# Optimization experiments

Hardware: AMD Instinct MI355X
Metric: run time of the kernel (lower is better)

## Reference

```python
import jax, jax.numpy as jnp
import numpy as np

KH, KW = 5, 5            # local window (h, w), must be odd
SIGMA = 1.0
GAUSS_DEN = 2.0 * SIGMA ** 2
N, C, H, W = 4, 20, 64, 2048


def setup_inputs() -> dict:
    key = jax.random.key(0)
    k1, k2, k3 = jax.random.split(key, 3)
    xyz = jax.random.normal(k1, (N, 3, H, W), dtype=jnp.float32)
    softmax = jax.random.uniform(k2, (N, C, H, W), dtype=jnp.float32)
    mask = jax.random.randint(k3, (N, H, W), 0, 2).astype(jnp.bool_)
    return {"xyz": xyz, "softmax": softmax, "mask": mask}


def reference(xyz, softmax, mask):
    # xyz: [N,3,H,W], softmax: [N,C,H,W], mask: [N,H,W]
    sm = softmax * mask[:, None].astype(softmax.dtype)
    ph, pw = KH // 2, KW // 2
    # zero padding matches F.unfold's implicit zero padding
    xyz_p = jnp.pad(xyz, ((0, 0), (0, 0), (ph, ph), (pw, pw)))
    sm_p = jnp.pad(sm, ((0, 0), (0, 0), (ph, ph), (pw, pw)))
    out = jnp.zeros_like(sm)
    # Fused form of the im2col math: for each window offset, weight the
    # shifted (masked) softmax by the XYZ-distance Gaussian and accumulate.
    # 25 static offsets -> small fixed unrolled loop, no giant unfold buffers.
    for dy in range(KH):
        for dx in range(KW):
            wxyz = xyz_p[:, :, dy:dy + sm.shape[2], dx:dx + sm.shape[3]]  # [N,3,H,W]
            d2 = jnp.sum((wxyz - xyz) ** 2, axis=1)                       # [N,H,W]
            g = jnp.exp(-d2 / GAUSS_DEN)                                  # [N,H,W]
            out = out + g[:, None] * sm_p[:, :, dy:dy + sm.shape[2], dx:dx + sm.shape[3]]
    return out
```

## Files before the change

kernel.cpp:

```cpp
#include <hip/hip_runtime.h>

#define NN 4
#define CC 20
#define HH 64
#define WW 2048
#define CG 4
#define CPG (CC / CG)
#define PX 4

__global__ __launch_bounds__(256, 4) void lc_xyz_kernel(
    const float* __restrict__ xyz,
    const float* __restrict__ softmax,
    const int* __restrict__ mask,
    float* __restrict__ out)
{
    const int t  = blockIdx.x * blockDim.x + threadIdx.x;
    const int h  = blockIdx.y;
    const int nz = blockIdx.z;
    const int n  = nz >> 2;
    const int cg = nz & 3;
    const int hw = HH * WW;
    const int p0 = t * PX;

    const float* xb  = xyz     + (size_t)n * 3  * hw;
    const float* smb = softmax + (size_t)n * CC * hw + (size_t)(cg * CPG) * hw;
    const int*   mb  = mask    + (size_t)n * hw;

    const int ctr = h * WW + p0;
    const float4 cxv = *(const float4*)(xb + 0 * hw + ctr);
    const float4 cyv = *(const float4*)(xb + 1 * hw + ctr);
    const float4 czv = *(const float4*)(xb + 2 * hw + ctr);
    const float cx[PX] = {cxv.x, cxv.y, cxv.z, cxv.w};
    const float cy[PX] = {cyv.x, cyv.y, cyv.z, cyv.w};
    const float cz[PX] = {czv.x, czv.y, czv.z, czv.w};

    float acc[CPG][PX];
#pragma unroll
    for (int c = 0; c < CPG; ++c)
#pragma unroll
        for (int i = 0; i < PX; ++i) acc[c][i] = 0.f;

    int c0 = p0 - 4; if (c0 < 0) c0 = 0;
    const int c1 = p0;
    int c2 = p0 + 4; if (c2 > WW - 4) c2 = WW - 4;

    float vf[12];
#pragma unroll
    for (int j = 2; j <= 9; ++j)
        vf[j] = ((unsigned)(p0 - 4 + j) < (unsigned)WW) ? 1.f : 0.f;

#pragma unroll
    for (int dy = -2; dy <= 2; ++dy) {
        const int row = h + dy;
        if ((unsigned)row >= (unsigned)HH) continue;
        const int rb = row * WW;

        const int4 m0 = *(const int4*)(mb + rb + c0);
        const int4 m1 = *(const int4*)(mb + rb + c1);
        const int4 m2 = *(const int4*)(mb + rb + c2);
        const float4 x0 = *(const float4*)(xb + 0 * hw + rb + c0);
        const float4 x1 = *(const float4*)(xb + 0 * hw + rb + c1);
        const float4 x2 = *(const float4*)(xb + 0 * hw + rb + c2);
        const float4 y0 = *(const float4*)(xb + 1 * hw + rb + c0);
        const float4 y1 = *(const float4*)(xb + 1 * hw + rb + c1);
        const float4 y2 = *(const float4*)(xb + 1 * hw + rb + c2);
        const float4 z0 = *(const float4*)(xb + 2 * hw + rb + c0);
        const float4 z1 = *(const float4*)(xb + 2 * hw + rb + c1);
        const float4 z2 = *(const float4*)(xb + 2 * hw + rb + c2);

        const float xw[12] = {x0.x,x0.y,x0.z,x0.w, x1.x,x1.y,x1.z,x1.w, x2.x,x2.y,x2.z,x2.w};
        const float yw[12] = {y0.x,y0.y,y0.z,y0.w, y1.x,y1.y,y1.z,y1.w, y2.x,y2.y,y2.z,y2.w};
        const float zw[12] = {z0.x,z0.y,z0.z,z0.w, z1.x,z1.y,z1.z,z1.w, z2.x,z2.y,z2.z,z2.w};
        const int   mi[12] = {m0.x,m0.y,m0.z,m0.w, m1.x,m1.y,m1.z,m1.w, m2.x,m2.y,m2.z,m2.w};

        float mf[12];
#pragma unroll
        for (int j = 2; j <= 9; ++j) mf[j] = vf[j] * (float)mi[j];

        float g[PX][5];
#pragma unroll
        for (int i = 0; i < PX; ++i) {
#pragma unroll
            for (int dx = 0; dx < 5; ++dx) {
                const int j = i + dx + 2;
                const float ax = xw[j] - cx[i];
                const float ay = yw[j] - cy[i];
                const float az = zw[j] - cz[i];
                const float d2 = ax * ax + ay * ay + az * az;
                g[i][dx] = mf[j] * __expf(-0.5f * d2);
            }
        }

#pragma unroll
        for (int c = 0; c < CPG; ++c) {
            const float* sp = smb + (size_t)c * hw + rb;
            const float4 s0 = *(const float4*)(sp + c0);
            const float4 s1 = *(const float4*)(sp + c1);
            const float4 s2 = *(const float4*)(sp + c2);
            const float sw[12] = {s0.x,s0.y,s0.z,s0.w, s1.x,s1.y,s1.z,s1.w, s2.x,s2.y,s2.z,s2.w};
#pragma unroll
            for (int i = 0; i < PX; ++i) {
                float a = acc[c][i];
#pragma unroll
                for (int dx = 0; dx < 5; ++dx)
                    a = fmaf(g[i][dx], sw[i + dx + 2], a);
                acc[c][i] = a;
            }
        }
    }

    float* ob = out + (size_t)n * CC * hw + (size_t)(cg * CPG) * hw + ctr;
#pragma unroll
    for (int c = 0; c < CPG; ++c)
        *(float4*)(ob + (size_t)c * hw) =
            make_float4(acc[c][0], acc[c][1], acc[c][2], acc[c][3]);
}

extern "C" void kernel_launch(void* const* d_in, const int* in_sizes, int n_in,
                              void* d_out, int out_size, void* d_ws, size_t ws_size,
                              hipStream_t stream) {
    const float* xyz     = (const float*)d_in[0];
    const float* softmax = (const float*)d_in[1];
    const int*   mask    = (const int*)d_in[2];
    float*       out     = (float*)d_out;

    dim3 block(256, 1, 1);
    dim3 grid(WW / (PX * 256), HH, NN * CG);
    hipLaunchKernelGGL(lc_xyz_kernel, grid, block, 0, stream,
                       xyz, softmax, mask, out);
}
```

Before: 132.5 us.

## Compute two output rows per thread to reuse loaded window rows

Each thread now produces two adjacent output rows, loading six input rows instead of five per output row, so softmax, xyz and mask loads are shared across rows. The grid is flattened to 1D with the n/channel-group index in the low bits, so the four channel groups and the batches are adjacent in launch order. Register pressure goes up (doubled accumulators and Gaussian weights), the launch bound drops to 3 waves per SIMD, and the block count halves, which may reduce occupancy.

```diff
diff --git a/kernel.cpp b/kernel.cpp
--- a/kernel.cpp
+++ b/kernel.cpp
@@ -7,38 +7,50 @@
 #define CG 4
 #define CPG (CC / CG)
 #define PX 4
+#define HT 2
 
-__global__ __launch_bounds__(256, 4) void lc_xyz_kernel(
+__global__ __launch_bounds__(256, 3) void lc_xyz_kernel(
     const float* __restrict__ xyz,
     const float* __restrict__ softmax,
     const int* __restrict__ mask,
     float* __restrict__ out)
 {
-    const int t  = blockIdx.x * blockDim.x + threadIdx.x;
-    const int h  = blockIdx.y;
-    const int nz = blockIdx.z;
-    const int n  = nz >> 2;
-    const int cg = nz & 3;
+    const int bid = blockIdx.x;
+    const int nz  = bid & 15;
+    const int r   = bid >> 4;
+    const int wb  = r & 1;
+    const int yb  = r >> 1;
+    const int n   = nz >> 2;
+    const int cg  = nz & 3;
+
     const int hw = HH * WW;
+    const int t  = wb * 256 + threadIdx.x;
     const int p0 = t * PX;
+    const int h0 = yb * HT;
 
     const float* xb  = xyz     + (size_t)n * 3  * hw;
     const float* smb = softmax + (size_t)n * CC * hw + (size_t)(cg * CPG) * hw;
     const int*   mb  = mask    + (size_t)n * hw;
 
-    const int ctr = h * WW + p0;
-    const float4 cxv = *(const float4*)(xb + 0 * hw + ctr);
-    const float4 cyv = *(const float4*)(xb + 1 * hw + ctr);
-    const float4 czv = *(const float4*)(xb + 2 * hw + ctr);
-    const float cx[PX] = {cxv.x, cxv.y, cxv.z, cxv.w};
-    const float cy[PX] = {cyv.x, cyv.y, cyv.z, cyv.w};
-    const float cz[PX] = {czv.x, czv.y, czv.z, czv.w};
+    float cx[HT][PX], cy[HT][PX], cz[HT][PX];
+#pragma unroll
+    for (int orow = 0; orow < HT; ++orow) {
+        const int ctr = (h0 + orow) * WW + p0;
+        const float4 a = *(const float4*)(xb + 0 * hw + ctr);
+        const float4 b = *(const float4*)(xb + 1 * hw + ctr);
+        const float4 c = *(const float4*)(xb + 2 * hw + ctr);
+        cx[orow][0]=a.x; cx[orow][1]=a.y; cx[orow][2]=a.z; cx[orow][3]=a.w;
+        cy[orow][0]=b.x; cy[orow][1]=b.y; cy[orow][2]=b.z; cy[orow][3]=b.w;
+        cz[orow][0]=c.x; cz[orow][1]=c.y; cz[orow][2]=c.z; cz[orow][3]=c.w;
+    }
 
-    float acc[CPG][PX];
+    float acc[CPG][HT][PX];
 #pragma unroll
     for (int c = 0; c < CPG; ++c)
 #pragma unroll
-        for (int i = 0; i < PX; ++i) acc[c][i] = 0.f;
+        for (int orow = 0; orow < HT; ++orow)
+#pragma unroll
+            for (int i = 0; i < PX; ++i) acc[c][orow][i] = 0.f;
 
     int c0 = p0 - 4; if (c0 < 0) c0 = 0;
     const int c1 = p0;
@@ -50,8 +62,8 @@
         vf[j] = ((unsigned)(p0 - 4 + j) < (unsigned)WW) ? 1.f : 0.f;
 
 #pragma unroll
-    for (int dy = -2; dy <= 2; ++dy) {
-        const int row = h + dy;
+    for (int k = 0; k < HT + 4; ++k) {
+        const int row = h0 - 2 + k;
         if ((unsigned)row >= (unsigned)HH) continue;
         const int rb = row * WW;
 
@@ -77,17 +89,21 @@
 #pragma unroll
         for (int j = 2; j <= 9; ++j) mf[j] = vf[j] * (float)mi[j];
 
-        float g[PX][5];
+        float g[HT][PX][5];
 #pragma unroll
-        for (int i = 0; i < PX; ++i) {
+        for (int orow = 0; orow < HT; ++orow) {
+            if (k < orow || k > orow + 4) continue;
 #pragma unroll
-            for (int dx = 0; dx < 5; ++dx) {
-                const int j = i + dx + 2;
-                const float ax = xw[j] - cx[i];
-                const float ay = yw[j] - cy[i];
-                const float az = zw[j] - cz[i];
-                const float d2 = ax * ax + ay * ay + az * az;
-                g[i][dx] = mf[j] * __expf(-0.5f * d2);
+            for (int i = 0; i < PX; ++i) {
+#pragma unroll
+                for (int dx = 0; dx < 5; ++dx) {
+                    const int j = i + dx + 2;
+                    const float ax = xw[j] - cx[orow][i];
+                    const float ay = yw[j] - cy[orow][i];
+                    const float az = zw[j] - cz[orow][i];
+                    const float d2 = ax * ax + ay * ay + az * az;
+                    g[orow][i][dx] = mf[j] * __expf(-0.5f * d2);
+                }
             }
         }
 
@@ -99,21 +115,30 @@
             const float4 s2 = *(const float4*)(sp + c2);
             const float sw[12] = {s0.x,s0.y,s0.z,s0.w, s1.x,s1.y,s1.z,s1.w, s2.x,s2.y,s2.z,s2.w};
 #pragma unroll
-            for (int i = 0; i < PX; ++i) {
-                float a = acc[c][i];
+            for (int orow = 0; orow < HT; ++orow) {
+                if (k < orow || k > orow + 4) continue;
 #pragma unroll
-                for (int dx = 0; dx < 5; ++dx)
-                    a = fmaf(g[i][dx], sw[i + dx + 2], a);
-                acc[c][i] = a;
+                for (int i = 0; i < PX; ++i) {
+                    float a = acc[c][orow][i];
+#pragma unroll
+                    for (int dx = 0; dx < 5; ++dx)
+                        a = fmaf(g[orow][i][dx], sw[i + dx + 2], a);
+                    acc[c][orow][i] = a;
+                }
             }
         }
     }
 
-    float* ob = out + (size_t)n * CC * hw + (size_t)(cg * CPG) * hw + ctr;
 #pragma unroll
-    for (int c = 0; c < CPG; ++c)
-        *(float4*)(ob + (size_t)c * hw) =
-            make_float4(acc[c][0], acc[c][1], acc[c][2], acc[c][3]);
+    for (int orow = 0; orow < HT; ++orow) {
+        float* ob = out + (size_t)n * CC * hw + (size_t)(cg * CPG) * hw
+                  + (h0 + orow) * WW + p0;
+#pragma unroll
+        for (int c = 0; c < CPG; ++c)
+            *(float4*)(ob + (size_t)c * hw) =
+                make_float4(acc[c][orow][0], acc[c][orow][1],
+                            acc[c][orow][2], acc[c][orow][3]);
+    }
 }
 
 extern "C" void kernel_launch(void* const* d_in, const int* in_sizes, int n_in,
@@ -125,7 +150,7 @@
     float*       out     = (float*)d_out;
 
     dim3 block(256, 1, 1);
-    dim3 grid(WW / (PX * 256), HH, NN * CG);
+    dim3 grid((WW / (PX * 256)) * (HH / HT) * NN * CG, 1, 1);
     hipLaunchKernelGGL(lc_xyz_kernel, grid, block, 0, stream,
                        xyz, softmax, mask, out);
 }
```

Result: slower. 159.7 us (+20.5%).

## Halve pixels per thread and remap blocks to a flat grid for locality

Applied to the files above, without the earlier changes.

Each thread now computes two pixels instead of four, doubling the number of threads and blocks, with float2 loads in place of float4. The grid is flattened to one dimension, ordered so that the 16 (batch, channel-group) blocks for the same row and width segment are adjacent. This is meant to raise occupancy and latency hiding and to improve cache reuse of the shared xyz and mask rows. In exchange, halo loads are amortised over fewer pixels, so more redundant loads and Gaussian computations are issued per output.

```diff
diff --git a/kernel.cpp b/kernel.cpp
--- a/kernel.cpp
+++ b/kernel.cpp
@@ -6,7 +6,7 @@
 #define WW 2048
 #define CG 4
 #define CPG (CC / CG)
-#define PX 4
+#define PX 2
 
 __global__ __launch_bounds__(256, 4) void lc_xyz_kernel(
     const float* __restrict__ xyz,
@@ -14,12 +14,16 @@
     const int* __restrict__ mask,
     float* __restrict__ out)
 {
-    const int t  = blockIdx.x * blockDim.x + threadIdx.x;
-    const int h  = blockIdx.y;
-    const int nz = blockIdx.z;
-    const int n  = nz >> 2;
-    const int cg = nz & 3;
+    const int bid = blockIdx.x;
+    const int nz  = bid & 15;
+    const int r   = bid >> 4;
+    const int wb  = r & 3;
+    const int h   = r >> 2;
+    const int n   = nz >> 2;
+    const int cg  = nz & 3;
+
     const int hw = HH * WW;
+    const int t  = wb * 256 + threadIdx.x;
     const int p0 = t * PX;
 
     const float* xb  = xyz     + (size_t)n * 3  * hw;
@@ -27,12 +31,12 @@
     const int*   mb  = mask    + (size_t)n * hw;
 
     const int ctr = h * WW + p0;
-    const float4 cxv = *(const float4*)(xb + 0 * hw + ctr);
-    const float4 cyv = *(const float4*)(xb + 1 * hw + ctr);
-    const float4 czv = *(const float4*)(xb + 2 * hw + ctr);
-    const float cx[PX] = {cxv.x, cxv.y, cxv.z, cxv.w};
-    const float cy[PX] = {cyv.x, cyv.y, cyv.z, cyv.w};
-    const float cz[PX] = {czv.x, czv.y, czv.z, czv.w};
+    const float2 cxv = *(const float2*)(xb + 0 * hw + ctr);
+    const float2 cyv = *(const float2*)(xb + 1 * hw + ctr);
+    const float2 czv = *(const float2*)(xb + 2 * hw + ctr);
+    const float cx[PX] = {cxv.x, cxv.y};
+    const float cy[PX] = {cyv.x, cyv.y};
+    const float cz[PX] = {czv.x, czv.y};
 
     float acc[CPG][PX];
 #pragma unroll
@@ -40,14 +44,14 @@
 #pragma unroll
         for (int i = 0; i < PX; ++i) acc[c][i] = 0.f;
 
-    int c0 = p0 - 4; if (c0 < 0) c0 = 0;
+    int c0 = p0 - 2; if (c0 < 0) c0 = 0;
     const int c1 = p0;
-    int c2 = p0 + 4; if (c2 > WW - 4) c2 = WW - 4;
+    int c2 = p0 + 2; if (c2 > WW - 2) c2 = WW - 2;
 
-    float vf[12];
+    float vf[6];
 #pragma unroll
-    for (int j = 2; j <= 9; ++j)
-        vf[j] = ((unsigned)(p0 - 4 + j) < (unsigned)WW) ? 1.f : 0.f;
+    for (int j = 0; j < 6; ++j)
+        vf[j] = ((unsigned)(p0 - 2 + j) < (unsigned)WW) ? 1.f : 0.f;
 
 #pragma unroll
     for (int dy = -2; dy <= 2; ++dy) {
@@ -55,34 +59,34 @@
         if ((unsigned)row >= (unsigned)HH) continue;
         const int rb = row * WW;
 
-        const int4 m0 = *(const int4*)(mb + rb + c0);
-        const int4 m1 = *(const int4*)(mb + rb + c1);
-        const int4 m2 = *(const int4*)(mb + rb + c2);
-        const float4 x0 = *(const float4*)(xb + 0 * hw + rb + c0);
-        const float4 x1 = *(const float4*)(xb + 0 * hw + rb + c1);
-        const float4 x2 = *(const float4*)(xb + 0 * hw + rb + c2);
-        const float4 y0 = *(const float4*)(xb + 1 * hw + rb + c0);
-        const float4 y1 = *(const float4*)(xb + 1 * hw + rb + c1);
-        const float4 y2 = *(const float4*)(xb + 1 * hw + rb + c2);
-        const float4 z0 = *(const float4*)(xb + 2 * hw + rb + c0);
-        const float4 z1 = *(const float4*)(xb + 2 * hw + rb + c1);
-        const float4 z2 = *(const float4*)(xb + 2 * hw + rb + c2);
+        const int2 m0 = *(const int2*)(mb + rb + c0);
+        const int2 m1 = *(const int2*)(mb + rb + c1);
+        const int2 m2 = *(const int2*)(mb + rb + c2);
+        const float2 x0 = *(const float2*)(xb + 0 * hw + rb + c0);
+        const float2 x1 = *(const float2*)(xb + 0 * hw + rb + c1);
+        const float2 x2 = *(const float2*)(xb + 0 * hw + rb + c2);
+        const float2 y0 = *(const float2*)(xb + 1 * hw + rb + c0);
+        const float2 y1 = *(const float2*)(xb + 1 * hw + rb + c1);
+        const float2 y2 = *(const float2*)(xb + 1 * hw + rb + c2);
+        const float2 z0 = *(const float2*)(xb + 2 * hw + rb + c0);
+        const float2 z1 = *(const float2*)(xb + 2 * hw + rb + c1);
+        const float2 z2 = *(const float2*)(xb + 2 * hw + rb + c2);
 
-        const float xw[12] = {x0.x,x0.y,x0.z,x0.w, x1.x,x1.y,x1.z,x1.w, x2.x,x2.y,x2.z,x2.w};
-        const float yw[12] = {y0.x,y0.y,y0.z,y0.w, y1.x,y1.y,y1.z,y1.w, y2.x,y2.y,y2.z,y2.w};
-        const float zw[12] = {z0.x,z0.y,z0.z,z0.w, z1.x,z1.y,z1.z,z1.w, z2.x,z2.y,z2.z,z2.w};
-        const int   mi[12] = {m0.x,m0.y,m0.z,m0.w, m1.x,m1.y,m1.z,m1.w, m2.x,m2.y,m2.z,m2.w};
+        const float xw[6] = {x0.x,x0.y, x1.x,x1.y, x2.x,x2.y};
+        const float yw[6] = {y0.x,y0.y, y1.x,y1.y, y2.x,y2.y};
+        const float zw[6] = {z0.x,z0.y, z1.x,z1.y, z2.x,z2.y};
+        const int   mi[6] = {m0.x,m0.y, m1.x,m1.y, m2.x,m2.y};
 
-        float mf[12];
+        float mf[6];
 #pragma unroll
-        for (int j = 2; j <= 9; ++j) mf[j] = vf[j] * (float)mi[j];
+        for (int j = 0; j < 6; ++j) mf[j] = vf[j] * (float)mi[j];
 
         float g[PX][5];
 #pragma unroll
         for (int i = 0; i < PX; ++i) {
 #pragma unroll
             for (int dx = 0; dx < 5; ++dx) {
-                const int j = i + dx + 2;
+                const int j = i + dx;
                 const float ax = xw[j] - cx[i];
                 const float ay = yw[j] - cy[i];
                 const float az = zw[j] - cz[i];
@@ -94,16 +98,16 @@
 #pragma unroll
         for (int c = 0; c < CPG; ++c) {
             const float* sp = smb + (size_t)c * hw + rb;
-            const float4 s0 = *(const float4*)(sp + c0);
-            const float4 s1 = *(const float4*)(sp + c1);
-            const float4 s2 = *(const float4*)(sp + c2);
-            const float sw[12] = {s0.x,s0.y,s0.z,s0.w, s1.x,s1.y,s1.z,s1.w, s2.x,s2.y,s2.z,s2.w};
+            const float2 s0 = *(const float2*)(sp + c0);
+            const float2 s1 = *(const float2*)(sp + c1);
+            const float2 s2 = *(const float2*)(sp + c2);
+            const float sw[6] = {s0.x,s0.y, s1.x,s1.y, s2.x,s2.y};
 #pragma unroll
             for (int i = 0; i < PX; ++i) {
                 float a = acc[c][i];
 #pragma unroll
                 for (int dx = 0; dx < 5; ++dx)
-                    a = fmaf(g[i][dx], sw[i + dx + 2], a);
+                    a = fmaf(g[i][dx], sw[i + dx], a);
                 acc[c][i] = a;
             }
         }
@@ -112,8 +116,7 @@
     float* ob = out + (size_t)n * CC * hw + (size_t)(cg * CPG) * hw + ctr;
 #pragma unroll
     for (int c = 0; c < CPG; ++c)
-        *(float4*)(ob + (size_t)c * hw) =
-            make_float4(acc[c][0], acc[c][1], acc[c][2], acc[c][3]);
+        *(float2*)(ob + (size_t)c * hw) = make_float2(acc[c][0], acc[c][1]);
 }
 
 extern "C" void kernel_launch(void* const* d_in, const int* in_sizes, int n_in,
@@ -125,7 +128,7 @@
     float*       out     = (float*)d_out;
 
     dim3 block(256, 1, 1);
-    dim3 grid(WW / (PX * 256), HH, NN * CG);
+    dim3 grid((WW / (PX * 256)) * HH * NN * CG, 1, 1);
     hipLaunchKernelGGL(lc_xyz_kernel, grid, block, 0, stream,
                        xyz, softmax, mask, out);
 }
```

Result: slower. 160.5 us (+21.1%).
